# Kernel tuning notes

Measured on AMD Instinct MI355X. Metric: run time of the kernel, lower is better.

Reference implementation:

```python
import jax, jax.numpy as jnp
import numpy as np

N_NODES = 100000
N_EDGES = 1600000
D_NODE = 384
HIDDEN = 64
LAYERS = 3


def setup_inputs() -> dict:
    key = jax.random.key(0)
    ks = jax.random.split(key, 10)
    x = jax.random.normal(ks[0], (N_NODES, D_NODE), dtype=jnp.float32)
    edge_index = jax.random.randint(ks[1], (2, N_EDGES), 0, N_NODES, dtype=jnp.int32)
    s = 0.05  # xavier-ish scale
    W_in = jax.random.normal(ks[2], (D_NODE, HIDDEN), dtype=jnp.float32) * s
    b_in = jnp.zeros((HIDDEN,), jnp.float32)
    Wl = jax.random.normal(ks[3], (LAYERS, HIDDEN, HIDDEN), dtype=jnp.float32) * s
    bl = jnp.zeros((LAYERS, HIDDEN), jnp.float32)
    Wr = jax.random.normal(ks[4], (LAYERS, HIDDEN, HIDDEN), dtype=jnp.float32) * s
    ln_g = jnp.ones((LAYERS, HIDDEN), jnp.float32)
    ln_b = jnp.zeros((LAYERS, HIDDEN), jnp.float32)
    out_g = jnp.ones((HIDDEN,), jnp.float32)
    out_b = jnp.zeros((HIDDEN,), jnp.float32)
    return {"x": x, "edge_index": edge_index, "W_in": W_in, "b_in": b_in,
            "Wl": Wl, "bl": bl, "Wr": Wr, "ln_g": ln_g, "ln_b": ln_b,
            "out_g": out_g, "out_b": out_b}


def _layer_norm(h, g, b, eps=1e-5):
    m = jnp.mean(h, axis=-1, keepdims=True)
    v = jnp.var(h, axis=-1, keepdims=True)
    return (h - m) * jax.lax.rsqrt(v + eps) * g + b


def reference(x, edge_index, W_in, b_in, Wl, bl, Wr, ln_g, ln_b, out_g, out_b):
    n = x.shape[0]
    src, dst = edge_index[0], edge_index[1]
    # input projection + relu (dropout is identity in eval)
    h = jax.nn.relu(x @ W_in + b_in)  # [N, H]
    # in-degree counts for mean aggregation (clamp to avoid div-by-zero)
    deg = jax.ops.segment_sum(jnp.ones_like(dst, dtype=h.dtype), dst, num_segments=n)
    deg = jnp.maximum(deg, 1.0)[:, None]  # [N, 1]
    for l in range(Wl.shape[0]):
        residual = h
        # SAGEConv: mean-aggregate neighbor features (gather + scatter-add)
        agg = jax.ops.segment_sum(h[src], dst, num_segments=n) / deg  # [N, H]
        out = agg @ Wl[l] + bl[l] + h @ Wr[l]
        # normalize=True -> L2 normalize rows
        out = out * jax.lax.rsqrt(jnp.maximum(jnp.sum(out * out, axis=-1, keepdims=True), 1e-24))
        out = jax.nn.relu(out)
        h = _layer_norm(out + residual, ln_g[l], ln_b[l])
    return _layer_norm(h, out_g, out_b)
```

## Files before the change

kernel.cpp:

```cpp
#include <hip/hip_runtime.h>

#define D_IN 384
#define HID 64
#define NLAYERS 3
#define KSTEPS_IN (D_IN / 32)
#define BKT_BITS 9
#define BKT_SIZE (1 << BKT_BITS)
#define BKT_CAP 12288
#define CHUNK 4096

typedef __attribute__((ext_vector_type(8))) short bf16x8;
typedef __attribute__((ext_vector_type(4))) float f32x4;
typedef __attribute__((ext_vector_type(4))) unsigned short us4;
typedef unsigned short u16;

__device__ __forceinline__ u16 f2bf(float f) {
    union { float f; unsigned u; } v; v.f = f;
    unsigned u = v.u;
    return (u16)((u + 0x7fffu + ((u >> 16) & 1u)) >> 16);
}
__device__ __forceinline__ float bf2f(u16 b) {
    union { unsigned u; float f; } v; v.u = ((unsigned)b) << 16;
    return v.f;
}

__global__ __launch_bounds__(256) void proj_mfma(const float* __restrict__ x,
                                                 const float* __restrict__ W,
                                                 const float* __restrict__ b,
                                                 u16* __restrict__ h, int N,
                                                 int* __restrict__ curA, int nbuk) {
    if (blockIdx.x == 0 && threadIdx.x < (unsigned)nbuk) curA[threadIdx.x] = 0;

    __shared__ u16 sB[KSTEPS_IN * 4 * 64 * 8];
    const int t = threadIdx.x;
    const int lane = t & 63;
    const int w = t >> 6;

    for (int fi = t; fi < KSTEPS_IN * 4 * 64; fi += 256) {
        int l  = fi & 63;
        int ct = (fi >> 6) & 3;
        int ks = fi >> 8;
        int kbase = ks * 32 + (l >> 4) * 8;
        int col   = ct * 16 + (l & 15);
        u16* d = &sB[(size_t)fi * 8];
        #pragma unroll
        for (int i = 0; i < 8; i++)
            d[i] = f2bf(W[(size_t)(kbase + i) * HID + col]);
    }
    __syncthreads();

    const int row0 = blockIdx.x * 256 + w * 64;
    f32x4 acc[4][4] = {};

    for (int ks = 0; ks < KSTEPS_IN; ks++) {
        bf16x8 a[4];
        #pragma unroll
        for (int rt = 0; rt < 4; rt++) {
            int row = row0 + rt * 16 + (lane & 15);
            if (row >= N) row = N - 1;
            const float* p = &x[(size_t)row * D_IN + ks * 32 + (lane >> 4) * 8];
            f32x4 x0 = *(const f32x4*)p;
            f32x4 x1 = *(const f32x4*)(p + 4);
            bf16x8 aa;
            aa[0] = (short)f2bf(x0[0]); aa[1] = (short)f2bf(x0[1]);
            aa[2] = (short)f2bf(x0[2]); aa[3] = (short)f2bf(x0[3]);
            aa[4] = (short)f2bf(x1[0]); aa[5] = (short)f2bf(x1[1]);
            aa[6] = (short)f2bf(x1[2]); aa[7] = (short)f2bf(x1[3]);
            a[rt] = aa;
        }
        #pragma unroll
        for (int ct = 0; ct < 4; ct++) {
            bf16x8 bb = *(const bf16x8*)&sB[(size_t)((ks * 4 + ct) * 64 + lane) * 8];
            #pragma unroll
            for (int rt = 0; rt < 4; rt++)
                acc[rt][ct] = __builtin_amdgcn_mfma_f32_16x16x32_bf16(a[rt], bb, acc[rt][ct], 0, 0, 0);
        }
    }

    float bias[4];
    #pragma unroll
    for (int ct = 0; ct < 4; ct++) bias[ct] = b[ct * 16 + (lane & 15)];

    #pragma unroll
    for (int rt = 0; rt < 4; rt++) {
        #pragma unroll
        for (int reg = 0; reg < 4; reg++) {
            int row = row0 + rt * 16 + (lane >> 4) * 4 + reg;
            if (row < N) {
                #pragma unroll
                for (int ct = 0; ct < 4; ct++) {
                    int col = ct * 16 + (lane & 15);
                    float v = acc[rt][ct][reg] + bias[ct];
                    h[(size_t)row * HID + col] = f2bf(fmaxf(v, 0.f));
                }
            }
        }
    }
}

__global__ __launch_bounds__(256) void phaseA(const int* __restrict__ src,
                                              const int* __restrict__ dst, int E,
                                              int* __restrict__ curA,
                                              unsigned* __restrict__ packed, int nbuk) {
    __shared__ int hist[256];
    __shared__ int sc[256];
    __shared__ int lbase[256];
    __shared__ int gbase[256];
    __shared__ int lcur[256];
    __shared__ unsigned buf[CHUNK];
    __shared__ unsigned char bid[CHUNK];
    const int t = threadIdx.x;
    const int e0 = blockIdx.x * CHUNK;
    const int cnt = min(CHUNK, E - e0);

    if (t < nbuk) hist[t] = 0;
    __syncthreads();

    unsigned pk[CHUNK / 256];
    int bk[CHUNK / 256];
    #pragma unroll
    for (int j = 0; j < CHUNK / 256; j++) {
        int idx = j * 256 + t;
        if (idx < cnt) {
            int e = e0 + idx;
            int d = dst[e];
            int s = src[e];
            bk[j] = d >> BKT_BITS;
            pk[j] = ((unsigned)s << BKT_BITS) | (unsigned)(d & (BKT_SIZE - 1));
            atomicAdd(&hist[bk[j]], 1);
        } else bk[j] = -1;
    }
    __syncthreads();
    sc[t] = (t < nbuk) ? hist[t] : 0;
    __syncthreads();
    for (int o = 1; o < 256; o <<= 1) {
        int v = (t >= o) ? sc[t - o] : 0;
        __syncthreads();
        sc[t] += v;
        __syncthreads();
    }
    if (t < nbuk) {
        lbase[t] = sc[t] - hist[t];
        lcur[t] = 0;
        gbase[t] = hist[t] ? (t * BKT_CAP + atomicAdd(&curA[t], hist[t])) : 0;
    }
    __syncthreads();
    #pragma unroll
    for (int j = 0; j < CHUNK / 256; j++) {
        if (bk[j] >= 0) {
            int r = atomicAdd(&lcur[bk[j]], 1);
            int slot = lbase[bk[j]] + r;
            buf[slot] = pk[j];
            bid[slot] = (unsigned char)bk[j];
        }
    }
    __syncthreads();
    for (int j = t; j < cnt; j += 256) {
        int b = bid[j];
        packed[gbase[b] + (j - lbase[b])] = buf[j];
    }
}

__global__ __launch_bounds__(256) void phaseB(const unsigned* __restrict__ packed,
                                              const int* __restrict__ curA,
                                              int N,
                                              int* __restrict__ ssorted,
                                              int4* __restrict__ meta) {
    __shared__ int ldeg[BKT_SIZE];
    __shared__ int s[BKT_SIZE];
    __shared__ int lcur[BKT_SIZE];
    const int b = blockIdx.x;
    const int t = threadIdx.x;
    const int rb = b * BKT_CAP;
    const int cnt = curA[b];
    for (int i = t; i < BKT_SIZE; i += 256) ldeg[i] = 0;
    __syncthreads();
    for (int j = t; j < cnt; j += 256)
        atomicAdd(&ldeg[packed[rb + j] & (BKT_SIZE - 1)], 1);
    __syncthreads();
    for (int i = t; i < BKT_SIZE; i += 256) s[i] = ldeg[i];
    __syncthreads();
    for (int o = 1; o < BKT_SIZE; o <<= 1) {
        int v0 = (t >= o) ? s[t - o] : 0;
        int i1 = t + 256;
        int v1 = (i1 >= o) ? s[i1 - o] : 0;
        __syncthreads();
        s[t] += v0;
        s[i1] += v1;
        __syncthreads();
    }
    const int n0 = b << BKT_BITS;
    for (int i = t; i < BKT_SIZE; i += 256) {
        int excl = (i == 0) ? 0 : s[i - 1];
        lcur[i] = excl;
        int n = n0 + i;
        if (n < N) {
            int4 m;
            m.x = rb + excl;
            m.y = rb + excl + ldeg[i];
            m.z = __float_as_int(1.0f / (float)max(ldeg[i], 1));
            m.w = 0;
            meta[n] = m;
        }
    }
    __syncthreads();
    for (int j = t; j < cnt; j += 256) {
        unsigned p = packed[rb + j];
        int l = p & (BKT_SIZE - 1);
        int r = atomicAdd(&lcur[l], 1);
        ssorted[rb + r] = (int)(p >> BKT_BITS);
    }
}

__global__ __launch_bounds__(256) void agg_kernel(const u16* __restrict__ h,
                                                  const int4* __restrict__ meta,
                                                  const int* __restrict__ ssorted,
                                                  u16* __restrict__ agg, int N) {
    const int lane = threadIdx.x & 63;
    const int wid  = (blockIdx.x * blockDim.x + threadIdx.x) >> 6;
    const int nw   = (gridDim.x * blockDim.x) >> 6;
    const int sub  = lane >> 4;
    const int cg   = lane & 15;
    for (int i = wid; i < N; i += nw) {
        const int4 m = meta[i];
        const int beg = m.x, end = m.y;
        float a0 = 0.f, a1 = 0.f, a2 = 0.f, a3 = 0.f;
        for (int e0 = beg; e0 < end; e0 += 16) {
            int e = e0 + sub;
            int j0 = e, j1 = e + 4, j2 = e + 8, j3 = e + 12;
            float p0 = (j0 < end) ? 1.f : 0.f;
            float p1 = (j1 < end) ? 1.f : 0.f;
            float p2 = (j2 < end) ? 1.f : 0.f;
            float p3 = (j3 < end) ? 1.f : 0.f;
            j0 = min(j0, end - 1); j1 = min(j1, end - 1);
            j2 = min(j2, end - 1); j3 = min(j3, end - 1);
            int s0 = ssorted[j0], s1 = ssorted[j1], s2 = ssorted[j2], s3 = ssorted[j3];
            us4 v0 = *(const us4*)&h[(size_t)s0 * HID + cg * 4];
            us4 v1 = *(const us4*)&h[(size_t)s1 * HID + cg * 4];
            us4 v2 = *(const us4*)&h[(size_t)s2 * HID + cg * 4];
            us4 v3 = *(const us4*)&h[(size_t)s3 * HID + cg * 4];
            a0 += p0 * bf2f(v0[0]) + p1 * bf2f(v1[0]) + p2 * bf2f(v2[0]) + p3 * bf2f(v3[0]);
            a1 += p0 * bf2f(v0[1]) + p1 * bf2f(v1[1]) + p2 * bf2f(v2[1]) + p3 * bf2f(v3[1]);
            a2 += p0 * bf2f(v0[2]) + p1 * bf2f(v1[2]) + p2 * bf2f(v2[2]) + p3 * bf2f(v3[2]);
            a3 += p0 * bf2f(v0[3]) + p1 * bf2f(v1[3]) + p2 * bf2f(v2[3]) + p3 * bf2f(v3[3]);
        }
        #pragma unroll
        for (int mm = 16; mm < 64; mm <<= 1) {
            a0 += __shfl_xor(a0, mm);
            a1 += __shfl_xor(a1, mm);
            a2 += __shfl_xor(a2, mm);
            a3 += __shfl_xor(a3, mm);
        }
        if (lane < 16) {
            float r = __int_as_float(m.z);
            us4 o;
            o[0] = f2bf(a0 * r); o[1] = f2bf(a1 * r);
            o[2] = f2bf(a2 * r); o[3] = f2bf(a3 * r);
            *(us4*)&agg[(size_t)i * HID + cg * 4] = o;
        }
    }
}

template<bool LAST>
__global__ __launch_bounds__(256) void layer_mfma(const u16* __restrict__ hin,
                                                  const u16* __restrict__ agg,
                                                  const float* __restrict__ Wl,
                                                  const float* __restrict__ Wr,
                                                  const float* __restrict__ bl,
                                                  const float* __restrict__ lng,
                                                  const float* __restrict__ lnb,
                                                  const float* __restrict__ og,
                                                  const float* __restrict__ ob,
                                                  u16* __restrict__ hout,
                                                  float* __restrict__ fout, int N) {
    __shared__ u16 sB[4 * 4 * 64 * 8];
    const int t = threadIdx.x;
    const int lane = t & 63;
    const int w = t >> 6;

    for (int fi = t; fi < 4 * 4 * 64; fi += 256) {
        int l  = fi & 63;
        int ct = (fi >> 6) & 3;
        int ks = fi >> 8;
        int kbase = ks * 32 + (l >> 4) * 8;
        int col   = ct * 16 + (l & 15);
        u16* d = &sB[(size_t)fi * 8];
        #pragma unroll
        for (int i = 0; i < 8; i++) {
            int kk = kbase + i;
            float wv = (kk < 64) ? Wl[(size_t)kk * HID + col]
                                 : Wr[(size_t)(kk - 64) * HID + col];
            d[i] = f2bf(wv);
        }
    }
    __syncthreads();

    const int row0 = blockIdx.x * 256 + w * 64;
    f32x4 acc[4][4] = {};

    #pragma unroll
    for (int ks = 0; ks < 4; ks++) {
        const u16* srcp = (ks < 2) ? agg : hin;
        const int ch0 = (ks & 1) * 32 + (lane >> 4) * 8;
        bf16x8 a[4];
        #pragma unroll
        for (int rt = 0; rt < 4; rt++) {
            int row = row0 + rt * 16 + (lane & 15);
            if (row >= N) row = N - 1;
            a[rt] = *(const bf16x8*)&srcp[(size_t)row * HID + ch0];
        }
        #pragma unroll
        for (int ct = 0; ct < 4; ct++) {
            bf16x8 bb = *(const bf16x8*)&sB[(size_t)((ks * 4 + ct) * 64 + lane) * 8];
            #pragma unroll
            for (int rt = 0; rt < 4; rt++)
                acc[rt][ct] = __builtin_amdgcn_mfma_f32_16x16x32_bf16(a[rt], bb, acc[rt][ct], 0, 0, 0);
        }
    }

    float bias[4], g4[4], be4[4], og4[4], ob4[4];
    #pragma unroll
    for (int ct = 0; ct < 4; ct++) {
        int c = ct * 16 + (lane & 15);
        bias[ct] = bl[c]; g4[ct] = lng[c]; be4[ct] = lnb[c];
        if (LAST) { og4[ct] = og[c]; ob4[ct] = ob[c]; }
    }

    #pragma unroll
    for (int rt = 0; rt < 4; rt++) {
        #pragma unroll
        for (int reg = 0; reg < 4; reg++) {
            int row = row0 + rt * 16 + (lane >> 4) * 4 + reg;
            if (row < N) {
                float v[4];
                float ss = 0.f;
                #pragma unroll
                for (int ct = 0; ct < 4; ct++) {
                    v[ct] = acc[rt][ct][reg] + bias[ct];
                    ss += v[ct] * v[ct];
                }
                #pragma unroll
                for (int m = 1; m < 16; m <<= 1) ss += __shfl_xor(ss, m);
                float rn = rsqrtf(fmaxf(ss, 1e-24f));
                float t4[4];
                float mean = 0.f;
                #pragma unroll
                for (int ct = 0; ct < 4; ct++) {
                    float o = fmaxf(v[ct] * rn, 0.f);
                    float hres = bf2f(hin[(size_t)row * HID + ct * 16 + (lane & 15)]);
                    t4[ct] = o + hres;
                    mean += t4[ct];
                }
                #pragma unroll
                for (int m = 1; m < 16; m <<= 1) mean += __shfl_xor(mean, m);
                mean *= (1.f / 64.f);
                float var = 0.f;
                #pragma unroll
                for (int ct = 0; ct < 4; ct++) {
                    float d = t4[ct] - mean;
                    var += d * d;
                }
                #pragma unroll
                for (int m = 1; m < 16; m <<= 1) var += __shfl_xor(var, m);
                var *= (1.f / 64.f);
                float rv = rsqrtf(var + 1e-5f);
                if (!LAST) {
                    #pragma unroll
                    for (int ct = 0; ct < 4; ct++)
                        hout[(size_t)row * HID + ct * 16 + (lane & 15)] =
                            f2bf((t4[ct] - mean) * rv * g4[ct] + be4[ct]);
                } else {
                    float y[4];
                    float m2 = 0.f;
                    #pragma unroll
                    for (int ct = 0; ct < 4; ct++) {
                        y[ct] = (t4[ct] - mean) * rv * g4[ct] + be4[ct];
                        m2 += y[ct];
                    }
                    #pragma unroll
                    for (int m = 1; m < 16; m <<= 1) m2 += __shfl_xor(m2, m);
                    m2 *= (1.f / 64.f);
                    float v2 = 0.f;
                    #pragma unroll
                    for (int ct = 0; ct < 4; ct++) {
                        float d = y[ct] - m2;
                        v2 += d * d;
                    }
                    #pragma unroll
                    for (int m = 1; m < 16; m <<= 1) v2 += __shfl_xor(v2, m);
                    v2 *= (1.f / 64.f);
                    float rv2 = rsqrtf(v2 + 1e-5f);
                    #pragma unroll
                    for (int ct = 0; ct < 4; ct++)
                        fout[(size_t)row * HID + ct * 16 + (lane & 15)] =
                            (y[ct] - m2) * rv2 * og4[ct] + ob4[ct];
                }
            }
        }
    }
}

extern "C" void kernel_launch(void* const* d_in, const int* in_sizes, int n_in,
                              void* d_out, int out_size, void* d_ws, size_t ws_size,
                              hipStream_t stream) {
    const float* x     = (const float*)d_in[0];
    const int*   ei    = (const int*)d_in[1];
    const float* W_in  = (const float*)d_in[2];
    const float* b_in  = (const float*)d_in[3];
    const float* Wl    = (const float*)d_in[4];
    const float* bl    = (const float*)d_in[5];
    const float* Wr    = (const float*)d_in[6];
    const float* ln_g  = (const float*)d_in[7];
    const float* ln_b  = (const float*)d_in[8];
    const float* out_g = (const float*)d_in[9];
    const float* out_b = (const float*)d_in[10];

    const int N = in_sizes[0] / D_IN;
    const int E = in_sizes[1] / 2;
    const int* src = ei;
    const int* dst = ei + E;
    const int nbuk = (N + BKT_SIZE - 1) >> BKT_BITS;

    char* ws = (char*)d_ws;
    size_t off = 0;
    auto take = [&](size_t bytes) {
        char* p = ws + off;
        off += (bytes + 255) & ~(size_t)255;
        return (void*)p;
    };
    u16*      h0      = (u16*)take((size_t)N * HID * 2);
    u16*      h1      = (u16*)take((size_t)N * HID * 2);
    u16*      aggb    = (u16*)take((size_t)N * HID * 2);
    int4*     meta    = (int4*)take((size_t)N * 16);
    int*      ssorted = (int*)take((size_t)nbuk * BKT_CAP * 4);
    unsigned* packedA = (unsigned*)take((size_t)nbuk * BKT_CAP * 4);
    int*      curA    = (int*)take((size_t)nbuk * 4);

    const int NBLK = (N + 255) / 256;

    proj_mfma<<<NBLK, 256, 0, stream>>>(x, W_in, b_in, h0, N, curA, nbuk);

    phaseA<<<(E + CHUNK - 1) / CHUNK, 256, 0, stream>>>(src, dst, E, curA, packedA, nbuk);
    phaseB<<<nbuk, 256, 0, stream>>>(packedA, curA, N, ssorted, meta);

    u16* hc = h0;
    u16* hn = h1;
    for (int l = 0; l < NLAYERS; l++) {
        agg_kernel<<<2048, 256, 0, stream>>>(hc, meta, ssorted, aggb, N);
        const float* wl = Wl + (size_t)l * HID * HID;
        const float* wr = Wr + (size_t)l * HID * HID;
        const float* bb = bl + (size_t)l * HID;
        const float* lg = ln_g + (size_t)l * HID;
        const float* lb = ln_b + (size_t)l * HID;
        if (l == NLAYERS - 1) {
            layer_mfma<true><<<NBLK, 256, 0, stream>>>(hc, aggb, wl, wr, bb, lg, lb,
                                                       out_g, out_b, nullptr,
                                                       (float*)d_out, N);
        } else {
            layer_mfma<false><<<NBLK, 256, 0, stream>>>(hc, aggb, wl, wr, bb, lg, lb,
                                                        nullptr, nullptr, hn, nullptr, N);
            u16* tmp = hc; hc = hn; hn = tmp;
        }
    }
}
```

Measured before the change: 264.9 us.

## Merge projection and edge bucketing into one launch; pad CSR rows for vector index loads

The input projection and the edge bucketing pass (phaseA) become one kernel that splits its blocks by block index, so the two independent jobs run at the same time and one launch is saved. curA is now zeroed with a memset. Each node's neighbour segment in the sorted edge array is padded to a multiple of 4, so the aggregation loop can fetch four source indices with one int4 load and skip predication on full 16-edge groups. The padding raises bucket occupancy, which shrinks the headroom under BKT_CAP, and the shared buffer sized for the larger branch may reduce occupancy for the projection blocks.

```diff
diff --git a/kernel.cpp b/kernel.cpp
--- a/kernel.cpp
+++ b/kernel.cpp
@@ -24,140 +24,140 @@
     return v.f;
 }
 
-__global__ __launch_bounds__(256) void proj_mfma(const float* __restrict__ x,
-                                                 const float* __restrict__ W,
-                                                 const float* __restrict__ b,
-                                                 u16* __restrict__ h, int N,
-                                                 int* __restrict__ curA, int nbuk) {
-    if (blockIdx.x == 0 && threadIdx.x < (unsigned)nbuk) curA[threadIdx.x] = 0;
-
-    __shared__ u16 sB[KSTEPS_IN * 4 * 64 * 8];
+__global__ __launch_bounds__(256) void proj_phaseA(const float* __restrict__ x,
+                                                   const float* __restrict__ W,
+                                                   const float* __restrict__ b,
+                                                   u16* __restrict__ h, int N, int nprojBlk,
+                                                   const int* __restrict__ src,
+                                                   const int* __restrict__ dst, int E,
+                                                   int* __restrict__ curA,
+                                                   unsigned* __restrict__ packed, int nbuk) {
+    __shared__ __align__(16) char smem[49152];
     const int t = threadIdx.x;
-    const int lane = t & 63;
-    const int w = t >> 6;
-
-    for (int fi = t; fi < KSTEPS_IN * 4 * 64; fi += 256) {
-        int l  = fi & 63;
-        int ct = (fi >> 6) & 3;
-        int ks = fi >> 8;
-        int kbase = ks * 32 + (l >> 4) * 8;
-        int col   = ct * 16 + (l & 15);
-        u16* d = &sB[(size_t)fi * 8];
-        #pragma unroll
-        for (int i = 0; i < 8; i++)
-            d[i] = f2bf(W[(size_t)(kbase + i) * HID + col]);
-    }
-    __syncthreads();
-
-    const int row0 = blockIdx.x * 256 + w * 64;
-    f32x4 acc[4][4] = {};
-
-    for (int ks = 0; ks < KSTEPS_IN; ks++) {
-        bf16x8 a[4];
+
+    if ((int)blockIdx.x < nprojBlk) {
+        u16* sB = (u16*)smem;
+        const int lane = t & 63;
+        const int w = t >> 6;
+
+        for (int fi = t; fi < KSTEPS_IN * 4 * 64; fi += 256) {
+            int l  = fi & 63;
+            int ct = (fi >> 6) & 3;
+            int ks = fi >> 8;
+            int kbase = ks * 32 + (l >> 4) * 8;
+            int col   = ct * 16 + (l & 15);
+            u16* d = &sB[(size_t)fi * 8];
+            #pragma unroll
+            for (int i = 0; i < 8; i++)
+                d[i] = f2bf(W[(size_t)(kbase + i) * HID + col]);
+        }
+        __syncthreads();
+
+        const int row0 = blockIdx.x * 256 + w * 64;
+        f32x4 acc[4][4] = {};
+
+        for (int ks = 0; ks < KSTEPS_IN; ks++) {
+            bf16x8 a[4];
+            #pragma unroll
+            for (int rt = 0; rt < 4; rt++) {
+                int row = row0 + rt * 16 + (lane & 15);
+                if (row >= N) row = N - 1;
+                const float* p = &x[(size_t)row * D_IN + ks * 32 + (lane >> 4) * 8];
+                f32x4 x0 = *(const f32x4*)p;
+                f32x4 x1 = *(const f32x4*)(p + 4);
+                bf16x8 aa;
+                aa[0] = (short)f2bf(x0[0]); aa[1] = (short)f2bf(x0[1]);
+                aa[2] = (short)f2bf(x0[2]); aa[3] = (short)f2bf(x0[3]);
+                aa[4] = (short)f2bf(x1[0]); aa[5] = (short)f2bf(x1[1]);
+                aa[6] = (short)f2bf(x1[2]); aa[7] = (short)f2bf(x1[3]);
+                a[rt] = aa;
+            }
+            #pragma unroll
+            for (int ct = 0; ct < 4; ct++) {
+                bf16x8 bb = *(const bf16x8*)&sB[(size_t)((ks * 4 + ct) * 64 + lane) * 8];
+                #pragma unroll
+                for (int rt = 0; rt < 4; rt++)
+                    acc[rt][ct] = __builtin_amdgcn_mfma_f32_16x16x32_bf16(a[rt], bb, acc[rt][ct], 0, 0, 0);
+            }
+        }
+
+        float bias[4];
+        #pragma unroll
+        for (int ct = 0; ct < 4; ct++) bias[ct] = b[ct * 16 + (lane & 15)];
+
         #pragma unroll
         for (int rt = 0; rt < 4; rt++) {
-            int row = row0 + rt * 16 + (lane & 15);
-            if (row >= N) row = N - 1;
-            const float* p = &x[(size_t)row * D_IN + ks * 32 + (lane >> 4) * 8];
-            f32x4 x0 = *(const f32x4*)p;
-            f32x4 x1 = *(const f32x4*)(p + 4);
-            bf16x8 aa;
-            aa[0] = (short)f2bf(x0[0]); aa[1] = (short)f2bf(x0[1]);
-            aa[2] = (short)f2bf(x0[2]); aa[3] = (short)f2bf(x0[3]);
-            aa[4] = (short)f2bf(x1[0]); aa[5] = (short)f2bf(x1[1]);
-            aa[6] = (short)f2bf(x1[2]); aa[7] = (short)f2bf(x1[3]);
-            a[rt] = aa;
-        }
-        #pragma unroll
-        for (int ct = 0; ct < 4; ct++) {
-            bf16x8 bb = *(const bf16x8*)&sB[(size_t)((ks * 4 + ct) * 64 + lane) * 8];
             #pragma unroll
-            for (int rt = 0; rt < 4; rt++)
-                acc[rt][ct] = __builtin_amdgcn_mfma_f32_16x16x32_bf16(a[rt], bb, acc[rt][ct], 0, 0, 0);
-        }
-    }
-
-    float bias[4];
-    #pragma unroll
-    for (int ct = 0; ct < 4; ct++) bias[ct] = b[ct * 16 + (lane & 15)];
-
-    #pragma unroll
-    for (int rt = 0; rt < 4; rt++) {
-        #pragma unroll
-        for (int reg = 0; reg < 4; reg++) {
-            int row = row0 + rt * 16 + (lane >> 4) * 4 + reg;
-            if (row < N) {
-                #pragma unroll
-                for (int ct = 0; ct < 4; ct++) {
-                    int col = ct * 16 + (lane & 15);
-                    float v = acc[rt][ct][reg] + bias[ct];
-                    h[(size_t)row * HID + col] = f2bf(fmaxf(v, 0.f));
+            for (int reg = 0; reg < 4; reg++) {
+                int row = row0 + rt * 16 + (lane >> 4) * 4 + reg;
+                if (row < N) {
+                    #pragma unroll
+                    for (int ct = 0; ct < 4; ct++) {
+                        int col = ct * 16 + (lane & 15);
+                        float v = acc[rt][ct][reg] + bias[ct];
+                        h[(size_t)row * HID + col] = f2bf(fmaxf(v, 0.f));
+                    }
                 }
             }
         }
-    }
-}
-
-__global__ __launch_bounds__(256) void phaseA(const int* __restrict__ src,
-                                              const int* __restrict__ dst, int E,
-                                              int* __restrict__ curA,
-                                              unsigned* __restrict__ packed, int nbuk) {
-    __shared__ int hist[256];
-    __shared__ int sc[256];
-    __shared__ int lbase[256];
-    __shared__ int gbase[256];
-    __shared__ int lcur[256];
-    __shared__ unsigned buf[CHUNK];
-    __shared__ unsigned char bid[CHUNK];
-    const int t = threadIdx.x;
-    const int e0 = blockIdx.x * CHUNK;
-    const int cnt = min(CHUNK, E - e0);
-
-    if (t < nbuk) hist[t] = 0;
-    __syncthreads();
-
-    unsigned pk[CHUNK / 256];
-    int bk[CHUNK / 256];
-    #pragma unroll
-    for (int j = 0; j < CHUNK / 256; j++) {
-        int idx = j * 256 + t;
-        if (idx < cnt) {
-            int e = e0 + idx;
-            int d = dst[e];
-            int s = src[e];
-            bk[j] = d >> BKT_BITS;
-            pk[j] = ((unsigned)s << BKT_BITS) | (unsigned)(d & (BKT_SIZE - 1));
-            atomicAdd(&hist[bk[j]], 1);
-        } else bk[j] = -1;
-    }
-    __syncthreads();
-    sc[t] = (t < nbuk) ? hist[t] : 0;
-    __syncthreads();
-    for (int o = 1; o < 256; o <<= 1) {
-        int v = (t >= o) ? sc[t - o] : 0;
-        __syncthreads();
-        sc[t] += v;
-        __syncthreads();
-    }
-    if (t < nbuk) {
-        lbase[t] = sc[t] - hist[t];
-        lcur[t] = 0;
-        gbase[t] = hist[t] ? (t * BKT_CAP + atomicAdd(&curA[t], hist[t])) : 0;
-    }
-    __syncthreads();
-    #pragma unroll
-    for (int j = 0; j < CHUNK / 256; j++) {
-        if (bk[j] >= 0) {
-            int r = atomicAdd(&lcur[bk[j]], 1);
-            int slot = lbase[bk[j]] + r;
-            buf[slot] = pk[j];
-            bid[slot] = (unsigned char)bk[j];
-        }
-    }
-    __syncthreads();
-    for (int j = t; j < cnt; j += 256) {
-        int b = bid[j];
-        packed[gbase[b] + (j - lbase[b])] = buf[j];
+    } else {
+        int* hist  = (int*)smem;
+        int* sc    = hist + 256;
+        int* lbase = sc + 256;
+        int* gbase = lbase + 256;
+        int* lcur  = gbase + 256;
+        unsigned* buf = (unsigned*)(lcur + 256);
+        unsigned char* bidA = (unsigned char*)(buf + CHUNK);
+        const int blk = blockIdx.x - nprojBlk;
+        const int e0 = blk * CHUNK;
+        const int cnt = min(CHUNK, E - e0);
+
+        if (t < nbuk) hist[t] = 0;
+        __syncthreads();
+
+        unsigned pk[CHUNK / 256];
+        int bk[CHUNK / 256];
+        #pragma unroll
+        for (int j = 0; j < CHUNK / 256; j++) {
+            int idx = j * 256 + t;
+            if (idx < cnt) {
+                int e = e0 + idx;
+                int d = dst[e];
+                int s = src[e];
+                bk[j] = d >> BKT_BITS;
+                pk[j] = ((unsigned)s << BKT_BITS) | (unsigned)(d & (BKT_SIZE - 1));
+                atomicAdd(&hist[bk[j]], 1);
+            } else bk[j] = -1;
+        }
+        __syncthreads();
+        sc[t] = (t < nbuk) ? hist[t] : 0;
+        __syncthreads();
+        for (int o = 1; o < 256; o <<= 1) {
+            int v = (t >= o) ? sc[t - o] : 0;
+            __syncthreads();
+            sc[t] += v;
+            __syncthreads();
+        }
+        if (t < nbuk) {
+            lbase[t] = sc[t] - hist[t];
+            lcur[t] = 0;
+            gbase[t] = hist[t] ? (t * BKT_CAP + atomicAdd(&curA[t], hist[t])) : 0;
+        }
+        __syncthreads();
+        #pragma unroll
+        for (int j = 0; j < CHUNK / 256; j++) {
+            if (bk[j] >= 0) {
+                int r = atomicAdd(&lcur[bk[j]], 1);
+                int slot = lbase[bk[j]] + r;
+                buf[slot] = pk[j];
+                bidA[slot] = (unsigned char)bk[j];
+            }
+        }
+        __syncthreads();
+        for (int j = t; j < cnt; j += 256) {
+            int bb2 = bidA[j];
+            packed[gbase[bb2] + (j - lbase[bb2])] = buf[j];
+        }
     }
 }
 
@@ -178,7 +178,7 @@
     for (int j = t; j < cnt; j += 256)
         atomicAdd(&ldeg[packed[rb + j] & (BKT_SIZE - 1)], 1);
     __syncthreads();
-    for (int i = t; i < BKT_SIZE; i += 256) s[i] = ldeg[i];
+    for (int i = t; i < BKT_SIZE; i += 256) s[i] = (ldeg[i] + 3) & ~3;
     __syncthreads();
     for (int o = 1; o < BKT_SIZE; o <<= 1) {
         int v0 = (t >= o) ? s[t - o] : 0;
@@ -191,13 +191,13 @@
     }
     const int n0 = b << BKT_BITS;
     for (int i = t; i < BKT_SIZE; i += 256) {
-        int excl = (i == 0) ? 0 : s[i - 1];
-        lcur[i] = excl;
+        int exclPad = (i == 0) ? 0 : s[i - 1];
+        lcur[i] = exclPad;
         int n = n0 + i;
         if (n < N) {
             int4 m;
-            m.x = rb + excl;
-            m.y = rb + excl + ldeg[i];
+            m.x = rb + exclPad;
+            m.y = rb + exclPad + ldeg[i];
             m.z = __float_as_int(1.0f / (float)max(ldeg[i], 1));
             m.w = 0;
             meta[n] = m;
@@ -225,16 +225,31 @@
         const int4 m = meta[i];
         const int beg = m.x, end = m.y;
         float a0 = 0.f, a1 = 0.f, a2 = 0.f, a3 = 0.f;
-        for (int e0 = beg; e0 < end; e0 += 16) {
-            int e = e0 + sub;
-            int j0 = e, j1 = e + 4, j2 = e + 8, j3 = e + 12;
+        int e0 = beg;
+        for (; e0 + 16 <= end; e0 += 16) {
+            const int lb = e0 + sub * 4;
+            int4 sidx = *(const int4*)&ssorted[lb];
+            us4 v0 = *(const us4*)&h[(size_t)sidx.x * HID + cg * 4];
+            us4 v1 = *(const us4*)&h[(size_t)sidx.y * HID + cg * 4];
+            us4 v2 = *(const us4*)&h[(size_t)sidx.z * HID + cg * 4];
+            us4 v3 = *(const us4*)&h[(size_t)sidx.w * HID + cg * 4];
+            a0 += bf2f(v0[0]) + bf2f(v1[0]) + bf2f(v2[0]) + bf2f(v3[0]);
+            a1 += bf2f(v0[1]) + bf2f(v1[1]) + bf2f(v2[1]) + bf2f(v3[1]);
+            a2 += bf2f(v0[2]) + bf2f(v1[2]) + bf2f(v2[2]) + bf2f(v3[2]);
+            a3 += bf2f(v0[3]) + bf2f(v1[3]) + bf2f(v2[3]) + bf2f(v3[3]);
+        }
+        if (e0 < end) {
+            const int lb = e0 + sub * 4;
+            int4 sidx = *(const int4*)&ssorted[lb];
+            int j0 = lb, j1 = lb + 1, j2 = lb + 2, j3 = lb + 3;
             float p0 = (j0 < end) ? 1.f : 0.f;
             float p1 = (j1 < end) ? 1.f : 0.f;
             float p2 = (j2 < end) ? 1.f : 0.f;
             float p3 = (j3 < end) ? 1.f : 0.f;
-            j0 = min(j0, end - 1); j1 = min(j1, end - 1);
-            j2 = min(j2, end - 1); j3 = min(j3, end - 1);
-            int s0 = ssorted[j0], s1 = ssorted[j1], s2 = ssorted[j2], s3 = ssorted[j3];
+            int s0 = (j0 < end) ? sidx.x : 0;
+            int s1 = (j1 < end) ? sidx.y : 0;
+            int s2 = (j2 < end) ? sidx.z : 0;
+            int s3 = (j3 < end) ? sidx.w : 0;
             us4 v0 = *(const us4*)&h[(size_t)s0 * HID + cg * 4];
             us4 v1 = *(const us4*)&h[(size_t)s1 * HID + cg * 4];
             us4 v2 = *(const us4*)&h[(size_t)s2 * HID + cg * 4];
@@ -432,15 +447,17 @@
     u16*      h1      = (u16*)take((size_t)N * HID * 2);
     u16*      aggb    = (u16*)take((size_t)N * HID * 2);
     int4*     meta    = (int4*)take((size_t)N * 16);
-    int*      ssorted = (int*)take((size_t)nbuk * BKT_CAP * 4);
-    unsigned* packedA = (unsigned*)take((size_t)nbuk * BKT_CAP * 4);
+    int*      ssorted = (int*)take(((size_t)nbuk * BKT_CAP + 64) * 4);
+    unsigned* packedA = (unsigned*)take(((size_t)nbuk * BKT_CAP + 64) * 4);
     int*      curA    = (int*)take((size_t)nbuk * 4);
 
     const int NBLK = (N + 255) / 256;
-
-    proj_mfma<<<NBLK, 256, 0, stream>>>(x, W_in, b_in, h0, N, curA, nbuk);
-
-    phaseA<<<(E + CHUNK - 1) / CHUNK, 256, 0, stream>>>(src, dst, E, curA, packedA, nbuk);
+    const int ABLK = (E + CHUNK - 1) / CHUNK;
+
+    hipMemsetAsync(curA, 0, (size_t)nbuk * 4, stream);
+    proj_phaseA<<<NBLK + ABLK, 256, 0, stream>>>(x, W_in, b_in, h0, N, NBLK,
+                                                 src, dst, E, curA, packedA, nbuk);
+
     phaseB<<<nbuk, 256, 0, stream>>>(packedA, curA, N, ssorted, meta);
 
     u16* hc = h0;
```

After: 255.8 us. 3.4% less time.
